# Kernel tuning notes

Measured on AMD Instinct MI355X. Metric: run time of the kernel, lower is better.

## Reference

```python
import jax, jax.numpy as jnp
import numpy as np

BINS = 64
VMIN, VMAX = 0.0, 1.0


def _calc_histogram(x):
    # x: [B, C, H, W] float
    B, C, H, W = x.shape
    x_norm = jnp.clip((x - VMIN) / (VMAX - VMIN), 0.0, 1.0)
    flat = x_norm.reshape(B * C, H * W)
    # torch.histc semantics over [0,1]: bin i = [i/BINS, (i+1)/BINS), last bin closed.
    idx = jnp.clip((flat * BINS).astype(jnp.int32), 0, BINS - 1)  # [B*C, HW]
    row_offset = (jnp.arange(B * C, dtype=jnp.int32) * BINS)[:, None]
    flat_idx = (idx + row_offset).reshape(-1)
    counts = jax.ops.segment_sum(
        jnp.ones(flat_idx.shape, dtype=x.dtype), flat_idx,
        num_segments=B * C * BINS,
    ).reshape(B * C, BINS)
    counts = counts / jnp.clip(counts.sum(axis=1, keepdims=True), 1e-8, None)
    return counts.reshape(B, C, BINS)


def reference(fake_images, real_images):
    hist_fake = _calc_histogram(fake_images)
    hist_real = _calc_histogram(real_images)
    # loss_type == 'l1'
    return jnp.abs(hist_fake - hist_real).mean()


def setup_inputs() -> dict:
    key = jax.random.key(0)
    k1, k2 = jax.random.split(key)
    shape = (32, 3, 512, 512)
    fake_images = jax.random.uniform(k1, shape, dtype=jnp.float32)
    real_images = jax.random.uniform(k2, shape, dtype=jnp.float32)
    return {"fake_images": fake_images, "real_images": real_images}
```

## Files before the change

kernel.cpp:

```cpp
#include <hip/hip_runtime.h>


#define HW        262144
#define ROWS      96
#define NBINS     64
#define BPR       8
#define CHUNK     (HW / BPR)
#define THREADS   256
#define F4_ITERS  (CHUNK / 4 / THREADS)
#define NBLOCKS   (2 * ROWS * BPR)

typedef unsigned long long u64;

__global__ __launch_bounds__(THREADS)
void hist_kernel(const float* __restrict__ fake,
                 const float* __restrict__ real,
                 unsigned int* __restrict__ partial) {
    __shared__ unsigned int bhist[NBINS];

    const int tid  = threadIdx.x;
    const int lane = tid & 63;

    if (tid < NBINS) bhist[tid] = 0u;
    __syncthreads();

    const int b     = blockIdx.x;
    const int chunk = b & (BPR - 1);
    const int rowg  = b >> 3;
    const float* src = (rowg < ROWS) ? fake : real;
    const int row    = (rowg < ROWS) ? rowg : (rowg - ROWS);

    const float4* __restrict__ p =
        (const float4*)(src + (size_t)row * HW + (size_t)chunk * CHUNK);

    u64 p0 = 0, p1 = 0, p2 = 0, p3 = 0, p4 = 0, p5 = 0, p6 = 0, p7 = 0;

#pragma unroll 4
    for (int i = 0; i < F4_ITERS; ++i) {
        float4 v = p[i * THREADS + tid];
        int b0 = min((int)(v.x * 64.0f), 63);
        int b1 = min((int)(v.y * 64.0f), 63);
        int b2 = min((int)(v.z * 64.0f), 63);
        int b3 = min((int)(v.w * 64.0f), 63);
        u64 m0 = 1ull << b0, m1 = 1ull << b1;
        u64 m2 = 1ull << b2, m3 = 1ull << b3;

        u64 s1 = m0 ^ m1, c1 = m0 & m1;
        u64 s2 = m2 ^ m3, c2 = m2 & m3;
        u64 S  = s1 ^ s2, C  = s1 & s2;

        u64 g0 = p0 & S;  p0 ^= S;

        u64 u  = c1 ^ c2, vv = c1 & c2;
        u64 s3 = u ^ C,   w  = u & C;
        u64 t3 = vv | w;

        u64 t  = s3 ^ g0;
        u64 g1 = (p1 & t) | (s3 & g0);
        p1 ^= t;

        u64 t2 = t3 ^ g1;
        u64 g2 = (p2 & t2) | (t3 & g1);
        p2 ^= t2;

        u64 g3 = p3 & g2; p3 ^= g2;
        u64 g4 = p4 & g3; p4 ^= g3;
        u64 g5 = p5 & g4; p5 ^= g4;
        u64 g6 = p6 & g5; p6 ^= g5;
        p7 ^= g6;
    }

    unsigned mycnt = 0;
#pragma unroll
    for (int bb = 0; bb < NBINS; ++bb) {
        unsigned ws =
              (unsigned)__popcll(__ballot((unsigned)((p0 >> bb) & 1ull)))
            + ((unsigned)__popcll(__ballot((unsigned)((p1 >> bb) & 1ull))) << 1)
            + ((unsigned)__popcll(__ballot((unsigned)((p2 >> bb) & 1ull))) << 2)
            + ((unsigned)__popcll(__ballot((unsigned)((p3 >> bb) & 1ull))) << 3)
            + ((unsigned)__popcll(__ballot((unsigned)((p4 >> bb) & 1ull))) << 4)
            + ((unsigned)__popcll(__ballot((unsigned)((p5 >> bb) & 1ull))) << 5)
            + ((unsigned)__popcll(__ballot((unsigned)((p6 >> bb) & 1ull))) << 6)
            + ((unsigned)__popcll(__ballot((unsigned)((p7 >> bb) & 1ull))) << 7);
        if (lane == bb) mycnt = ws;
    }
    atomicAdd(&bhist[lane], mycnt);
    __syncthreads();

    if (tid < NBINS)
        partial[(size_t)b * NBINS + tid] = bhist[tid];
}

__global__ __launch_bounds__(1024)
void loss_kernel(const unsigned int* __restrict__ partial,
                 float* __restrict__ out) {
    const int tid = threadIdx.x;
    int acc = 0;
#pragma unroll
    for (int q = 0; q < 6; ++q) {
        const int pIdx = q * 1024 + tid;
        const int r  = pIdx >> 6;
        const int bb = pIdx & 63;
        unsigned cf = 0, cr = 0;
#pragma unroll
        for (int c = 0; c < BPR; ++c) {
            cf += partial[((r * BPR + c) * NBINS) + bb];
            cr += partial[(((ROWS + r) * BPR + c) * NBINS) + bb];
        }
        int d = (int)cf - (int)cr;
        acc += (d < 0) ? -d : d;
    }
#pragma unroll
    for (int off = 32; off > 0; off >>= 1)
        acc += __shfl_down(acc, off, 64);
    __shared__ int wsum[16];
    if ((tid & 63) == 0) wsum[tid >> 6] = acc;
    __syncthreads();
    if (tid == 0) {
        long long total = 0;
#pragma unroll
        for (int k = 0; k < 16; ++k) total += wsum[k];
        out[0] = (float)((double)total / (262144.0 * 6144.0));
    }
}

extern "C" void kernel_launch(void* const* d_in, const int* in_sizes, int n_in,
                              void* d_out, int out_size, void* d_ws, size_t ws_size,
                              hipStream_t stream) {
    const float* fake = (const float*)d_in[0];
    const float* real = (const float*)d_in[1];
    unsigned int* partial = (unsigned int*)d_ws;
    float* out = (float*)d_out;

    hist_kernel<<<NBLOCKS, THREADS, 0, stream>>>(fake, real, partial);
    loss_kernel<<<1, 1024, 0, stream>>>(partial, out);
}
```

Measured before the change: 228.5 us.

## Halve blocks per row, prefetch loads in registers, split loss reduction

Each histogram block now covers twice as many elements (BPR 8 to 4), so a thread's bit-sliced counters must reach 256 counts and a ninth counter plane is added. The main loop software-pipelines four float4 loads ahead of the bit-sliced processing and sets launch bounds to request occupancy of three blocks. The single-block loss kernel is split into a 24-block partial reduction and a tiny final reduction. The aim is to hide memory latency and cut per-block setup and ballot overhead, at the cost of an extra kernel launch and more registers per thread.

```diff
diff --git a/kernel.cpp b/kernel.cpp
--- a/kernel.cpp
+++ b/kernel.cpp
@@ -4,7 +4,7 @@
 #define HW        262144
 #define ROWS      96
 #define NBINS     64
-#define BPR       8
+#define BPR       4
 #define CHUNK     (HW / BPR)
 #define THREADS   256
 #define F4_ITERS  (CHUNK / 4 / THREADS)
@@ -12,7 +12,33 @@
 
 typedef unsigned long long u64;
 
-__global__ __launch_bounds__(THREADS)
+#define PROC4(v) do {                                                   \
+    int b0 = min((int)((v).x * 64.0f), 63);                             \
+    int b1 = min((int)((v).y * 64.0f), 63);                             \
+    int b2 = min((int)((v).z * 64.0f), 63);                             \
+    int b3 = min((int)((v).w * 64.0f), 63);                             \
+    u64 m0 = 1ull << b0, m1 = 1ull << b1;                               \
+    u64 m2 = 1ull << b2, m3 = 1ull << b3;                               \
+    u64 s1 = m0 ^ m1, c1 = m0 & m1;                                     \
+    u64 s2 = m2 ^ m3, c2 = m2 & m3;                                     \
+    u64 S  = s1 ^ s2, C  = s1 & s2;                                     \
+    u64 g0 = p0 & S;  p0 ^= S;                                          \
+    u64 u  = c1 ^ c2, vv = c1 & c2;                                     \
+    u64 s3 = u ^ C,   w  = u & C;                                       \
+    u64 t3 = vv | w;                                                    \
+    u64 t  = s3 ^ g0;                                                   \
+    u64 g1 = (p1 & t) | (s3 & g0);  p1 ^= t;                            \
+    u64 t2 = t3 ^ g1;                                                   \
+    u64 g2 = (p2 & t2) | (t3 & g1); p2 ^= t2;                           \
+    u64 g3 = p3 & g2; p3 ^= g2;                                         \
+    u64 g4 = p4 & g3; p4 ^= g3;                                         \
+    u64 g5 = p5 & g4; p5 ^= g4;                                         \
+    u64 g6 = p6 & g5; p6 ^= g5;                                         \
+    u64 g7 = p7 & g6; p7 ^= g6;                                         \
+    p8 ^= g7;                                                           \
+} while (0)
+
+__global__ __launch_bounds__(THREADS, 3)
 void hist_kernel(const float* __restrict__ fake,
                  const float* __restrict__ real,
                  unsigned int* __restrict__ partial) {
@@ -26,49 +52,28 @@
 
     const int b     = blockIdx.x;
     const int chunk = b & (BPR - 1);
-    const int rowg  = b >> 3;
+    const int rowg  = b >> 2;
     const float* src = (rowg < ROWS) ? fake : real;
     const int row    = (rowg < ROWS) ? rowg : (rowg - ROWS);
 
-    const float4* __restrict__ p =
-        (const float4*)(src + (size_t)row * HW + (size_t)chunk * CHUNK);
+    const float4* __restrict__ q =
+        (const float4*)(src + (size_t)row * HW + (size_t)chunk * CHUNK) + tid;
 
-    u64 p0 = 0, p1 = 0, p2 = 0, p3 = 0, p4 = 0, p5 = 0, p6 = 0, p7 = 0;
+    u64 p0 = 0, p1 = 0, p2 = 0, p3 = 0, p4 = 0, p5 = 0, p6 = 0, p7 = 0, p8 = 0;
 
-#pragma unroll 4
-    for (int i = 0; i < F4_ITERS; ++i) {
-        float4 v = p[i * THREADS + tid];
-        int b0 = min((int)(v.x * 64.0f), 63);
-        int b1 = min((int)(v.y * 64.0f), 63);
-        int b2 = min((int)(v.z * 64.0f), 63);
-        int b3 = min((int)(v.w * 64.0f), 63);
-        u64 m0 = 1ull << b0, m1 = 1ull << b1;
-        u64 m2 = 1ull << b2, m3 = 1ull << b3;
-
-        u64 s1 = m0 ^ m1, c1 = m0 & m1;
-        u64 s2 = m2 ^ m3, c2 = m2 & m3;
-        u64 S  = s1 ^ s2, C  = s1 & s2;
-
-        u64 g0 = p0 & S;  p0 ^= S;
-
-        u64 u  = c1 ^ c2, vv = c1 & c2;
-        u64 s3 = u ^ C,   w  = u & C;
-        u64 t3 = vv | w;
-
-        u64 t  = s3 ^ g0;
-        u64 g1 = (p1 & t) | (s3 & g0);
-        p1 ^= t;
-
-        u64 t2 = t3 ^ g1;
-        u64 g2 = (p2 & t2) | (t3 & g1);
-        p2 ^= t2;
-
-        u64 g3 = p3 & g2; p3 ^= g2;
-        u64 g4 = p4 & g3; p4 ^= g3;
-        u64 g5 = p5 & g4; p5 ^= g4;
-        u64 g6 = p6 & g5; p6 ^= g5;
-        p7 ^= g6;
+    float4 c0 = q[0 * THREADS];
+    float4 c1 = q[1 * THREADS];
+    float4 c2 = q[2 * THREADS];
+    float4 c3 = q[3 * THREADS];
+    for (int i = 4; i < F4_ITERS; i += 4) {
+        float4 n0 = q[(i + 0) * THREADS];
+        float4 n1 = q[(i + 1) * THREADS];
+        float4 n2 = q[(i + 2) * THREADS];
+        float4 n3 = q[(i + 3) * THREADS];
+        PROC4(c0); PROC4(c1); PROC4(c2); PROC4(c3);
+        c0 = n0; c1 = n1; c2 = n2; c3 = n3;
     }
+    PROC4(c0); PROC4(c1); PROC4(c2); PROC4(c3);
 
     unsigned mycnt = 0;
 #pragma unroll
@@ -81,7 +86,8 @@
             + ((unsigned)__popcll(__ballot((unsigned)((p4 >> bb) & 1ull))) << 4)
             + ((unsigned)__popcll(__ballot((unsigned)((p5 >> bb) & 1ull))) << 5)
             + ((unsigned)__popcll(__ballot((unsigned)((p6 >> bb) & 1ull))) << 6)
-            + ((unsigned)__popcll(__ballot((unsigned)((p7 >> bb) & 1ull))) << 7);
+            + ((unsigned)__popcll(__ballot((unsigned)((p7 >> bb) & 1ull))) << 7)
+            + ((unsigned)__popcll(__ballot((unsigned)((p8 >> bb) & 1ull))) << 8);
         if (lane == bb) mycnt = ws;
     }
     atomicAdd(&bhist[lane], mycnt);
@@ -91,37 +97,41 @@
         partial[(size_t)b * NBINS + tid] = bhist[tid];
 }
 
-__global__ __launch_bounds__(1024)
-void loss_kernel(const unsigned int* __restrict__ partial,
-                 float* __restrict__ out) {
+__global__ __launch_bounds__(256)
+void loss1_kernel(const unsigned int* __restrict__ partial,
+                  unsigned int* __restrict__ blocksum) {
     const int tid = threadIdx.x;
-    int acc = 0;
+    const int g   = blockIdx.x * 256 + tid;
+    const int r   = g >> 6;
+    const int bb  = g & 63;
+    unsigned cf = 0, cr = 0;
 #pragma unroll
-    for (int q = 0; q < 6; ++q) {
-        const int pIdx = q * 1024 + tid;
-        const int r  = pIdx >> 6;
-        const int bb = pIdx & 63;
-        unsigned cf = 0, cr = 0;
-#pragma unroll
-        for (int c = 0; c < BPR; ++c) {
-            cf += partial[((r * BPR + c) * NBINS) + bb];
-            cr += partial[(((ROWS + r) * BPR + c) * NBINS) + bb];
-        }
-        int d = (int)cf - (int)cr;
-        acc += (d < 0) ? -d : d;
+    for (int c = 0; c < BPR; ++c) {
+        cf += partial[((r * BPR + c) * NBINS) + bb];
+        cr += partial[(((ROWS + r) * BPR + c) * NBINS) + bb];
     }
+    int d = (int)cf - (int)cr;
+    int a = (d < 0) ? -d : d;
 #pragma unroll
     for (int off = 32; off > 0; off >>= 1)
-        acc += __shfl_down(acc, off, 64);
-    __shared__ int wsum[16];
-    if ((tid & 63) == 0) wsum[tid >> 6] = acc;
+        a += __shfl_down(a, off, 64);
+    __shared__ int wsum[4];
+    if ((tid & 63) == 0) wsum[tid >> 6] = a;
     __syncthreads();
-    if (tid == 0) {
-        long long total = 0;
+    if (tid == 0)
+        blocksum[blockIdx.x] = (unsigned)(wsum[0] + wsum[1] + wsum[2] + wsum[3]);
+}
+
+__global__ __launch_bounds__(64)
+void loss2_kernel(const unsigned int* __restrict__ blocksum,
+                  float* __restrict__ out) {
+    const int lane = threadIdx.x;
+    int a = (lane < 24) ? (int)blocksum[lane] : 0;
 #pragma unroll
-        for (int k = 0; k < 16; ++k) total += wsum[k];
-        out[0] = (float)((double)total / (262144.0 * 6144.0));
-    }
+    for (int off = 32; off > 0; off >>= 1)
+        a += __shfl_down(a, off, 64);
+    if (lane == 0)
+        out[0] = (float)((double)a / (262144.0 * 6144.0));
 }
 
 extern "C" void kernel_launch(void* const* d_in, const int* in_sizes, int n_in,
@@ -129,9 +139,11 @@
                               hipStream_t stream) {
     const float* fake = (const float*)d_in[0];
     const float* real = (const float*)d_in[1];
-    unsigned int* partial = (unsigned int*)d_ws;
+    unsigned int* partial  = (unsigned int*)d_ws;
+    unsigned int* blocksum = partial + NBLOCKS * NBINS;
     float* out = (float*)d_out;
 
     hist_kernel<<<NBLOCKS, THREADS, 0, stream>>>(fake, real, partial);
-    loss_kernel<<<1, 1024, 0, stream>>>(partial, out);
+    loss1_kernel<<<24, 256, 0, stream>>>(partial, blocksum);
+    loss2_kernel<<<1, 64, 0, stream>>>(blocksum, out);
 }
```

Result: no change. 228.5 us (-0.0%).
